# Kernel tuning notes

Measured on AMD Instinct MI355X. Metric: run time of the kernel, lower is better.

The kernel has to match this reference:

```python
import jax, jax.numpy as jnp
import numpy as np

N_NODES = 207
N_EDGES = 1722
N_SLOTS = 288  # 288 / resolution with resolution = 1


def setup_inputs() -> dict:
    key = jax.random.key(0)
    ks = jax.random.split(key, 7)
    B, C, L = 1024, 2, 64
    inputs = jax.random.normal(ks[0], (B, C, N_NODES, L), dtype=jnp.float32)
    weight_diff = jax.random.normal(ks[1], (N_SLOTS, N_EDGES), dtype=jnp.float32) / 1000.0
    bias_diffusion = jax.random.normal(ks[2], (N_SLOTS, N_NODES), dtype=jnp.float32) / 10.0
    weight_self_loop = jax.random.normal(ks[3], (N_SLOTS, N_NODES), dtype=jnp.float32) / 10.0
    ind = jax.random.randint(ks[4], (B,), 0, N_SLOTS, dtype=jnp.int32)
    edge_i = jax.random.randint(ks[5], (N_EDGES,), 0, N_NODES, dtype=jnp.int32)
    edge_j = jax.random.randint(ks[6], (N_EDGES,), 0, N_NODES, dtype=jnp.int32)
    return {"inputs": inputs, "weight_diff": weight_diff,
            "bias_diffusion": bias_diffusion, "weight_self_loop": weight_self_loop,
            "ind": ind, "edge_i": edge_i, "edge_j": edge_j}


def reference(inputs, weight_diff, bias_diffusion, weight_self_loop, ind, edge_i, edge_j):
    # resolution = 1 -> slot index ii == ind
    x = inputs[:, 0, :, :]                      # [B, N, L]
    B, N, _ = x.shape
    w = weight_diff[ind]                        # [B, E] per-sample edge weights
    # symmetric scatter into batched dense adjacency (duplicates sum, as in sparse_coo_tensor)
    A = jnp.zeros((B, N, N), dtype=x.dtype)
    A = A.at[:, edge_i, edge_j].add(w).at[:, edge_j, edge_i].add(w)
    deg = jnp.sum(A, axis=1)                    # [B, N]  (sum over dim 1, as in torch code)
    lap = deg[:, :, None] * jnp.eye(N, dtype=x.dtype) - A  # L = diag(deg) - A
    diffusion = jnp.einsum('nvl,nwv->nwl', x, lap) + bias_diffusion[ind][:, :, None]
    self_loop = weight_self_loop[ind][:, :, None] * x
    return diffusion + x + self_loop
```

## Files before the change

### kernel.cpp

```cpp
#include <hip/hip_runtime.h>
#include <stdint.h>

#define N_NODES 207
#define N_EDGES 1722
#define N_SLOTS 288
#define L_DIM   64
#define EB_STRIDE 4096

__device__ __forceinline__ unsigned int f2bf_rtn_bits_hi(float f) {
    unsigned int u = __float_as_uint(f);
    unsigned int r = u + 0x7FFFu + ((u >> 16) & 1u);
    return r & 0xFFFF0000u;
}

__global__ __launch_bounds__(256) void build_csr_kernel(
    const int* __restrict__ edge_i, const int* __restrict__ edge_j,
    int* __restrict__ rs_p, unsigned int* __restrict__ csr_p) {
    __shared__ int cnt[N_NODES];
    __shared__ int rs[N_NODES + 1];
    const int tid = threadIdx.x;

    for (int n = tid; n < N_NODES; n += 256) cnt[n] = 0;
    __syncthreads();
    for (int e = tid; e < N_EDGES; e += 256) {
        atomicAdd(&cnt[edge_i[e]], 1);
        atomicAdd(&cnt[edge_j[e]], 1);
    }
    __syncthreads();
    if (tid == 0) {
        int acc = 0;
        for (int n = 0; n < N_NODES; ++n) { rs[n] = acc; acc += (cnt[n] + 3) & ~3; }
        rs[N_NODES] = acc;
    }
    __syncthreads();
    for (int n = tid; n <= N_NODES; n += 256) rs_p[n] = rs[n];
    for (int k = tid; k < EB_STRIDE; k += 256) csr_p[k] = 0xFFFFFFFFu;
    for (int n = tid; n < N_NODES; n += 256) cnt[n] = rs[n];
    __syncthreads();
    for (int e = tid; e < N_EDGES; e += 256) {
        const unsigned int i = edge_i[e], j = edge_j[e];
        const unsigned int ep = ((unsigned int)e) << 8;
        int p = atomicAdd(&cnt[i], 1);
        csr_p[p] = ep | j;
        int q = atomicAdd(&cnt[j], 1);
        csr_p[q] = ep | i;
    }
}

__global__ __launch_bounds__(256) void coef_eb_kernel(
    const float* __restrict__ weight_diff, const float* __restrict__ bias_diffusion,
    const float* __restrict__ weight_self_loop,
    const int* __restrict__ rs_p, const unsigned int* __restrict__ csr_p,
    float2* __restrict__ coefbias, unsigned int* __restrict__ eb32p) {
    __shared__ float wrow[N_EDGES];
    const int s = blockIdx.x;
    for (int e = threadIdx.x; e < N_EDGES; e += 256)
        wrow[e] = weight_diff[(size_t)s * N_EDGES + e];
    __syncthreads();

    if (eb32p != nullptr) {
        const int EP = rs_p[N_NODES];
        unsigned int* ebs = eb32p + (size_t)s * EB_STRIDE;
        for (int k = threadIdx.x; k < EB_STRIDE; k += 256) {
            unsigned int v = 0u;
            if (k < EP) {
                const unsigned int c = csr_p[k];
                if (c != 0xFFFFFFFFu)
                    v = f2bf_rtn_bits_hi(wrow[c >> 8]) | ((c & 255u) << 7);
            }
            ebs[k] = v;
        }
    }

    const int n = threadIdx.x;
    if (n < N_NODES) {
        float d = 0.f;
        const int e0 = rs_p[n], e1 = rs_p[n + 1];
        for (int k = e0; k < e1; ++k) {
            const unsigned int c = csr_p[k];
            if (c != 0xFFFFFFFFu) d += wrow[c >> 8];
        }
        coefbias[s * N_NODES + n] = make_float2(
            1.f + weight_self_loop[s * N_NODES + n] + d,
            bias_diffusion[s * N_NODES + n]);
    }
}

__global__ __launch_bounds__(512, 8) void diffusion_quad_kernel(
    const float* __restrict__ inputs,
    const int*   __restrict__ ind,
    const int*   __restrict__ rs_p_g,
    const unsigned int* __restrict__ eb32p,
    const float2* __restrict__ coefbias,
    float* __restrict__ out) {
    __shared__ unsigned short xs[N_NODES * L_DIM];
    __shared__ unsigned int   rsp[N_NODES];

    const int b    = blockIdx.x;
    const int tid  = threadIdx.x;
    const int slot = ind[b];

    const float* xb = inputs + (size_t)b * (2 * N_NODES * L_DIM);

    const float4* xb4 = (const float4*)xb;
    for (int k = tid; k < (N_NODES * L_DIM) / 4; k += 512) {
        const float4 v = xb4[k];
        const unsigned int lo = (f2bf_rtn_bits_hi(v.x) >> 16) | f2bf_rtn_bits_hi(v.y);
        const unsigned int hi = (f2bf_rtn_bits_hi(v.z) >> 16) | f2bf_rtn_bits_hi(v.w);
        ((uint2*)xs)[k] = make_uint2(lo, hi);
    }
    for (int n = tid; n < N_NODES; n += 512)
        rsp[n] = (unsigned int)rs_p_g[n] | ((unsigned int)rs_p_g[n + 1] << 16);
    __syncthreads();

    const int lane = tid & 63;
    const int wv   = tid >> 6;
    const int h    = lane >> 4;
    const unsigned int li8 = (unsigned int)((lane & 15) << 3);
    const unsigned int* ebs = eb32p + (size_t)slot * EB_STRIDE;
    const float2* cbs = coefbias + (size_t)slot * N_NODES;
    float* ob = out + (size_t)b * (N_NODES * L_DIM);
    const char* xsb = (const char*)xs;

    for (int n = wv; n < N_NODES; n += 8) {
        const unsigned int rr = rsp[n];
        const int e0 = (int)(rr & 0xFFFFu);
        const int e1 = (int)(rr >> 16);
        float s0 = 0.f, s1 = 0.f, s2 = 0.f, s3 = 0.f;
        #pragma unroll 2
        for (int k = e0; k < e1; k += 4) {
            const unsigned int p = ebs[k + h];
            const unsigned int w = p & 0xFFFF0000u;
            const unsigned int off = (p & 0xFFFFu) | li8;
            const uint2 xv = *(const uint2*)(xsb + off);
            s0 = fmaf(__uint_as_float(w), __uint_as_float(xv.x << 16), s0);
            s1 = fmaf(__uint_as_float(w), __uint_as_float(xv.x & 0xFFFF0000u), s1);
            s2 = fmaf(__uint_as_float(w), __uint_as_float(xv.y << 16), s2);
            s3 = fmaf(__uint_as_float(w), __uint_as_float(xv.y & 0xFFFF0000u), s3);
        }
        s0 += __shfl_xor(s0, 16); s1 += __shfl_xor(s1, 16);
        s2 += __shfl_xor(s2, 16); s3 += __shfl_xor(s3, 16);
        s0 += __shfl_xor(s0, 32); s1 += __shfl_xor(s1, 32);
        s2 += __shfl_xor(s2, 32); s3 += __shfl_xor(s3, 32);
        if (lane < 16) {
            const float2 cb = cbs[n];
            const int o4 = (n << 6) + (lane << 2);
            const float4 xg = *(const float4*)(xb + o4);
            float4 o;
            o.x = fmaf(cb.x, xg.x, cb.y) - s0;
            o.y = fmaf(cb.x, xg.y, cb.y) - s1;
            o.z = fmaf(cb.x, xg.z, cb.y) - s2;
            o.w = fmaf(cb.x, xg.w, cb.y) - s3;
            *(float4*)(ob + o4) = o;
        }
    }
}

__global__ __launch_bounds__(512, 8) void diffusion_gcn_fallback(
    const float* __restrict__ inputs,
    const float* __restrict__ weight_diff,
    const int*   __restrict__ ind,
    const int*   __restrict__ rs_p_g,
    const unsigned int* __restrict__ csr_p,
    const float2* __restrict__ coefbias,
    float* __restrict__ out) {
    __shared__ unsigned short xsh[N_NODES * L_DIM];
    __shared__ unsigned int   wnb[EB_STRIDE];
    __shared__ unsigned short rs[N_NODES + 1];

    const int b    = blockIdx.x;
    const int tid  = threadIdx.x;
    const int slot = ind[b];

    const float* xb = inputs + (size_t)b * (2 * N_NODES * L_DIM);

    const float4* xb4 = (const float4*)xb;
    for (int k = tid; k < (N_NODES * L_DIM) / 4; k += 512) {
        const float4 v = xb4[k];
        const unsigned int lo = (f2bf_rtn_bits_hi(v.x) >> 16) | f2bf_rtn_bits_hi(v.y);
        const unsigned int hi = (f2bf_rtn_bits_hi(v.z) >> 16) | f2bf_rtn_bits_hi(v.w);
        ((uint2*)xsh)[k] = make_uint2(lo, hi);
    }
    const int EP = rs_p_g[N_NODES];
    const float* wrow = weight_diff + (size_t)slot * N_EDGES;
    for (int k = tid; k < EP; k += 512) {
        const unsigned int c = csr_p[k];
        wnb[k] = (c == 0xFFFFFFFFu) ? 0u
                                    : (f2bf_rtn_bits_hi(wrow[c >> 8]) | (c & 255u));
    }
    for (int n = tid; n <= N_NODES; n += 512) rs[n] = (unsigned short)rs_p_g[n];
    __syncthreads();

    const int lane = tid & 63;
    const int wv   = tid >> 6;
    float* ob = out + (size_t)b * (N_NODES * L_DIM);

    for (int n = wv; n < N_NODES; n += 8) {
        const int e0 = rs[n], e1 = rs[n + 1];
        float s = 0.f;
        #pragma unroll 4
        for (int k = e0; k < e1; ++k) {
            const unsigned int p = wnb[k];
            const float w  = __uint_as_float(p & 0xFFFF0000u);
            const float xv = __uint_as_float(
                (unsigned int)xsh[(p & 255u) * L_DIM + lane] << 16);
            s = fmaf(w, xv, s);
        }
        const float2 cb = coefbias[slot * N_NODES + n];
        const float  xg = xb[n * L_DIM + lane];
        ob[n * L_DIM + lane] = fmaf(cb.x, xg, cb.y) - s;
    }
}

extern "C" void kernel_launch(void* const* d_in, const int* in_sizes, int n_in,
                              void* d_out, int out_size, void* d_ws, size_t ws_size,
                              hipStream_t stream) {
    const float* inputs           = (const float*)d_in[0];
    const float* weight_diff      = (const float*)d_in[1];
    const float* bias_diffusion   = (const float*)d_in[2];
    const float* weight_self_loop = (const float*)d_in[3];
    const int*   ind              = (const int*)d_in[4];
    const int*   edge_i           = (const int*)d_in[5];
    const int*   edge_j           = (const int*)d_in[6];
    float* out = (float*)d_out;

    const int B = in_sizes[4];

    char* ws = (char*)d_ws;
    int*          rs_p     = (int*)ws;
    unsigned int* csr_p    = (unsigned int*)(ws + 1024);
    float2*       coefbias = (float2*)(ws + 17408);
    unsigned int* eb32p    = (unsigned int*)(ws + 494336);
    const size_t WS_FULL = 494336 + (size_t)N_SLOTS * EB_STRIDE * sizeof(unsigned int);

    const bool full = (d_ws != nullptr) && (ws_size >= WS_FULL);

    build_csr_kernel<<<1, 256, 0, stream>>>(edge_i, edge_j, rs_p, csr_p);
    coef_eb_kernel<<<N_SLOTS, 256, 0, stream>>>(
        weight_diff, bias_diffusion, weight_self_loop, rs_p, csr_p,
        coefbias, full ? eb32p : nullptr);
    if (full) {
        diffusion_quad_kernel<<<B, 512, 0, stream>>>(
            inputs, ind, rs_p, eb32p, coefbias, out);
    } else {
        diffusion_gcn_fallback<<<B, 512, 0, stream>>>(
            inputs, weight_diff, ind, rs_p, csr_p, coefbias, out);
    }
}
```

Before: 238.4 us.

## Keep node features in fp32 shared memory and use packed-FMA accumulation

The diffusion kernel now stages the input slice in shared memory as fp32 instead of converting it to bf16. Neighbor rows are read as float4, and accumulation uses 2-wide float vectors so the compiler can emit packed FMA. The edge-buffer node offset is shifted to match the 16-byte row stride. The epilogue also reads x from shared memory instead of global. This removes the bf16 conversion and unpacking ALU work and improves accuracy. In exchange it doubles LDS use (about 53 KB per block), lowers the occupancy hint from 8 to 6, and doubles LDS read bandwidth per edge.

```diff
diff --git a/kernel.cpp b/kernel.cpp
--- a/kernel.cpp
+++ b/kernel.cpp
@@ -6,6 +6,8 @@
 #define N_SLOTS 288
 #define L_DIM   64
 #define EB_STRIDE 4096
+
+typedef __attribute__((ext_vector_type(2))) float f32x2;
 
 __device__ __forceinline__ unsigned int f2bf_rtn_bits_hi(float f) {
     unsigned int u = __float_as_uint(f);
@@ -66,7 +68,7 @@
             if (k < EP) {
                 const unsigned int c = csr_p[k];
                 if (c != 0xFFFFFFFFu)
-                    v = f2bf_rtn_bits_hi(wrow[c >> 8]) | ((c & 255u) << 7);
+                    v = f2bf_rtn_bits_hi(wrow[c >> 8]) | ((c & 255u) << 8);
             }
             ebs[k] = v;
         }
@@ -86,15 +88,15 @@
     }
 }
 
-__global__ __launch_bounds__(512, 8) void diffusion_quad_kernel(
+__global__ __launch_bounds__(512, 6) void diffusion_quad32_kernel(
     const float* __restrict__ inputs,
     const int*   __restrict__ ind,
     const int*   __restrict__ rs_p_g,
     const unsigned int* __restrict__ eb32p,
     const float2* __restrict__ coefbias,
     float* __restrict__ out) {
-    __shared__ unsigned short xs[N_NODES * L_DIM];
-    __shared__ unsigned int   rsp[N_NODES];
+    __shared__ float        xs[N_NODES * L_DIM];
+    __shared__ unsigned int rsp[N_NODES];
 
     const int b    = blockIdx.x;
     const int tid  = threadIdx.x;
@@ -103,12 +105,8 @@
     const float* xb = inputs + (size_t)b * (2 * N_NODES * L_DIM);
 
     const float4* xb4 = (const float4*)xb;
-    for (int k = tid; k < (N_NODES * L_DIM) / 4; k += 512) {
-        const float4 v = xb4[k];
-        const unsigned int lo = (f2bf_rtn_bits_hi(v.x) >> 16) | f2bf_rtn_bits_hi(v.y);
-        const unsigned int hi = (f2bf_rtn_bits_hi(v.z) >> 16) | f2bf_rtn_bits_hi(v.w);
-        ((uint2*)xs)[k] = make_uint2(lo, hi);
-    }
+    float4* xs4 = (float4*)xs;
+    for (int k = tid; k < (N_NODES * L_DIM) / 4; k += 512) xs4[k] = xb4[k];
     for (int n = tid; n < N_NODES; n += 512)
         rsp[n] = (unsigned int)rs_p_g[n] | ((unsigned int)rs_p_g[n + 1] << 16);
     __syncthreads();
@@ -116,8 +114,8 @@
     const int lane = tid & 63;
     const int wv   = tid >> 6;
     const int h    = lane >> 4;
-    const unsigned int li8 = (unsigned int)((lane & 15) << 3);
-    const unsigned int* ebs = eb32p + (size_t)slot * EB_STRIDE;
+    const unsigned int li16 = (unsigned int)((lane & 15) << 4);
+    const unsigned int* ebs = eb32p + (size_t)slot * EB_STRIDE + h;
     const float2* cbs = coefbias + (size_t)slot * N_NODES;
     float* ob = out + (size_t)b * (N_NODES * L_DIM);
     const char* xsb = (const char*)xs;
@@ -126,18 +124,20 @@
         const unsigned int rr = rsp[n];
         const int e0 = (int)(rr & 0xFFFFu);
         const int e1 = (int)(rr >> 16);
-        float s0 = 0.f, s1 = 0.f, s2 = 0.f, s3 = 0.f;
+        f32x2 sA = {0.f, 0.f}, sB = {0.f, 0.f};
         #pragma unroll 2
         for (int k = e0; k < e1; k += 4) {
-            const unsigned int p = ebs[k + h];
-            const unsigned int w = p & 0xFFFF0000u;
-            const unsigned int off = (p & 0xFFFFu) | li8;
-            const uint2 xv = *(const uint2*)(xsb + off);
-            s0 = fmaf(__uint_as_float(w), __uint_as_float(xv.x << 16), s0);
-            s1 = fmaf(__uint_as_float(w), __uint_as_float(xv.x & 0xFFFF0000u), s1);
-            s2 = fmaf(__uint_as_float(w), __uint_as_float(xv.y << 16), s2);
-            s3 = fmaf(__uint_as_float(w), __uint_as_float(xv.y & 0xFFFF0000u), s3);
-        }
+            const unsigned int p = ebs[k];
+            const float w = __uint_as_float(p & 0xFFFF0000u);
+            const unsigned int off = (p & 0xFFFFu) | li16;
+            const float4 xv = *(const float4*)(xsb + off);
+            const f32x2 w2 = {w, w};
+            const f32x2 xlo = {xv.x, xv.y};
+            const f32x2 xhi = {xv.z, xv.w};
+            sA += w2 * xlo;
+            sB += w2 * xhi;
+        }
+        float s0 = sA.x, s1 = sA.y, s2 = sB.x, s3 = sB.y;
         s0 += __shfl_xor(s0, 16); s1 += __shfl_xor(s1, 16);
         s2 += __shfl_xor(s2, 16); s3 += __shfl_xor(s3, 16);
         s0 += __shfl_xor(s0, 32); s1 += __shfl_xor(s1, 32);
@@ -145,7 +145,7 @@
         if (lane < 16) {
             const float2 cb = cbs[n];
             const int o4 = (n << 6) + (lane << 2);
-            const float4 xg = *(const float4*)(xb + o4);
+            const float4 xg = *(const float4*)(xs + o4);
             float4 o;
             o.x = fmaf(cb.x, xg.x, cb.y) - s0;
             o.y = fmaf(cb.x, xg.y, cb.y) - s1;
@@ -240,7 +240,7 @@
         weight_diff, bias_diffusion, weight_self_loop, rs_p, csr_p,
         coefbias, full ? eb32p : nullptr);
     if (full) {
-        diffusion_quad_kernel<<<B, 512, 0, stream>>>(
+        diffusion_quad32_kernel<<<B, 512, 0, stream>>>(
             inputs, ind, rs_p, eb32p, coefbias, out);
     } else {
         diffusion_gcn_fallback<<<B, 512, 0, stream>>>(
```

Result: slower. 255.1 us (+7.0%).

## Flatten per-wave edge groups with shared-memory bf16 weights and topology

Applied to the files above, without the earlier changes.

Builds a per-wave flattened edge layout in which nodes are padded to groups of four and assigned round-robin to the eight waves. A node-id array marks group boundaries. Per-slot weights are stored as 16-bit bf16 values, separate from an 8-bit neighbor topology array. The diffusion kernel stages weights, topology and node ids into LDS and runs one continuous loop per wave, reducing and writing output whenever the node changes. This aims to remove per-node loop overhead and the global 32-bit edge-word loads, at the cost of more LDS use (which may lower occupancy) and a divergent reduction branch inside the inner loop.

```diff
diff --git a/kernel.cpp b/kernel.cpp
--- a/kernel.cpp
+++ b/kernel.cpp
@@ -5,19 +5,27 @@
 #define N_EDGES 1722
 #define N_SLOTS 288
 #define L_DIM   64
-#define EB_STRIDE 4096
+#define CSRP_CAP 4096
+#define WSTR_CAP 4608
+#define W16_STRIDE 4608
+#define NGRP_CAP 1280
 
 __device__ __forceinline__ unsigned int f2bf_rtn_bits_hi(float f) {
     unsigned int u = __float_as_uint(f);
     unsigned int r = u + 0x7FFFu + ((u >> 16) & 1u);
     return r & 0xFFFF0000u;
 }
+__device__ __forceinline__ float uf(unsigned int u) { return __uint_as_float(u); }
 
 __global__ __launch_bounds__(256) void build_csr_kernel(
     const int* __restrict__ edge_i, const int* __restrict__ edge_j,
-    int* __restrict__ rs_p, unsigned int* __restrict__ csr_p) {
+    int* __restrict__ rs_p, unsigned int* __restrict__ csr_p,
+    unsigned int* __restrict__ csr_w, unsigned char* __restrict__ topo8,
+    unsigned char* __restrict__ nodearr, int* __restrict__ wvoff) {
     __shared__ int cnt[N_NODES];
     __shared__ int rs[N_NODES + 1];
+    __shared__ int nbase[N_NODES];
+    __shared__ int ngsz[N_NODES];
     const int tid = threadIdx.x;
 
     for (int n = tid; n < N_NODES; n += 256) cnt[n] = 0;
@@ -34,7 +42,7 @@
     }
     __syncthreads();
     for (int n = tid; n <= N_NODES; n += 256) rs_p[n] = rs[n];
-    for (int k = tid; k < EB_STRIDE; k += 256) csr_p[k] = 0xFFFFFFFFu;
+    for (int k = tid; k < CSRP_CAP; k += 256) csr_p[k] = 0xFFFFFFFFu;
     for (int n = tid; n < N_NODES; n += 256) cnt[n] = rs[n];
     __syncthreads();
     for (int e = tid; e < N_EDGES; e += 256) {
@@ -45,30 +53,65 @@
         int q = atomicAdd(&cnt[j], 1);
         csr_p[q] = ep | i;
     }
+    __syncthreads();
+    if (tid == 0) {
+        int wsz[8] = {0,0,0,0,0,0,0,0};
+        for (int n = 0; n < N_NODES; ++n) {
+            int dp = rs[n + 1] - rs[n];
+            int g = (dp > 4) ? dp : 4;
+            ngsz[n] = g;
+            wsz[n & 7] += g;
+        }
+        int acc = 0, wo[9];
+        for (int w = 0; w < 8; ++w) { wo[w] = acc; acc += wsz[w]; }
+        wo[8] = acc;
+        for (int w = 0; w <= 8; ++w) wvoff[w] = wo[w];
+        int cur[8];
+        for (int w = 0; w < 8; ++w) cur[w] = wo[w];
+        for (int n = 0; n < N_NODES; ++n) {
+            const int w = n & 7;
+            nbase[n] = cur[w];
+            cur[w] += ngsz[n];
+        }
+        nodearr[acc >> 2] = 0xFFu;
+    }
+    __syncthreads();
+    for (int n = tid; n < N_NODES; n += 256) {
+        const int b0 = nbase[n], dp = rs[n + 1] - rs[n], g = ngsz[n];
+        for (int i = 0; i < dp; ++i) {
+            const unsigned int c = csr_p[rs[n] + i];
+            csr_w[b0 + i] = c;
+            topo8[b0 + i] = (unsigned char)(c & 255u);
+        }
+        for (int i = dp; i < g; ++i) {
+            csr_w[b0 + i] = 0xFFFFFFFFu;
+            topo8[b0 + i] = 0;
+        }
+        const int G = g >> 2, gb = b0 >> 2;
+        for (int j = 0; j < G; ++j) nodearr[gb + j] = (unsigned char)n;
+    }
 }
 
 __global__ __launch_bounds__(256) void coef_eb_kernel(
     const float* __restrict__ weight_diff, const float* __restrict__ bias_diffusion,
     const float* __restrict__ weight_self_loop,
     const int* __restrict__ rs_p, const unsigned int* __restrict__ csr_p,
-    float2* __restrict__ coefbias, unsigned int* __restrict__ eb32p) {
+    const unsigned int* __restrict__ csr_w, const int* __restrict__ wvoff,
+    float2* __restrict__ coefbias, unsigned short* __restrict__ w16) {
     __shared__ float wrow[N_EDGES];
     const int s = blockIdx.x;
     for (int e = threadIdx.x; e < N_EDGES; e += 256)
         wrow[e] = weight_diff[(size_t)s * N_EDGES + e];
     __syncthreads();
 
-    if (eb32p != nullptr) {
-        const int EP = rs_p[N_NODES];
-        unsigned int* ebs = eb32p + (size_t)s * EB_STRIDE;
-        for (int k = threadIdx.x; k < EB_STRIDE; k += 256) {
-            unsigned int v = 0u;
-            if (k < EP) {
-                const unsigned int c = csr_p[k];
-                if (c != 0xFFFFFFFFu)
-                    v = f2bf_rtn_bits_hi(wrow[c >> 8]) | ((c & 255u) << 7);
-            }
-            ebs[k] = v;
+    if (w16 != nullptr) {
+        const int total = wvoff[8];
+        unsigned short* ws = w16 + (size_t)s * W16_STRIDE;
+        for (int k = threadIdx.x; k < total; k += 256) {
+            const unsigned int c = csr_w[k];
+            ws[k] = (c == 0xFFFFFFFFu)
+                  ? (unsigned short)0
+                  : (unsigned short)(f2bf_rtn_bits_hi(wrow[c >> 8]) >> 16);
         }
     }
 
@@ -86,19 +129,24 @@
     }
 }
 
-__global__ __launch_bounds__(512, 8) void diffusion_quad_kernel(
+__global__ __launch_bounds__(512, 8) void diffusion_flat_kernel(
     const float* __restrict__ inputs,
     const int*   __restrict__ ind,
-    const int*   __restrict__ rs_p_g,
-    const unsigned int* __restrict__ eb32p,
+    const int*   __restrict__ wvoff,
+    const unsigned char*  __restrict__ topo8,
+    const unsigned char*  __restrict__ nodearr,
+    const unsigned short* __restrict__ w16,
     const float2* __restrict__ coefbias,
     float* __restrict__ out) {
     __shared__ unsigned short xs[N_NODES * L_DIM];
-    __shared__ unsigned int   rsp[N_NODES];
+    __shared__ unsigned short ws16[WSTR_CAP - 256];
+    __shared__ unsigned char  tp[WSTR_CAP - 256];
+    __shared__ unsigned char  ndl[1152];
 
     const int b    = blockIdx.x;
     const int tid  = threadIdx.x;
     const int slot = ind[b];
+    const int total = wvoff[8];
 
     const float* xb = inputs + (size_t)b * (2 * N_NODES * L_DIM);
 
@@ -109,54 +157,65 @@
         const unsigned int hi = (f2bf_rtn_bits_hi(v.z) >> 16) | f2bf_rtn_bits_hi(v.w);
         ((uint2*)xs)[k] = make_uint2(lo, hi);
     }
-    for (int n = tid; n < N_NODES; n += 512)
-        rsp[n] = (unsigned int)rs_p_g[n] | ((unsigned int)rs_p_g[n + 1] << 16);
+    {
+        const unsigned int* wg = (const unsigned int*)(w16 + (size_t)slot * W16_STRIDE);
+        for (int k = tid; k < (total >> 1); k += 512) ((unsigned int*)ws16)[k] = wg[k];
+        const unsigned int* tg = (const unsigned int*)topo8;
+        for (int k = tid; k < (total >> 2); k += 512) ((unsigned int*)tp)[k] = tg[k];
+        const unsigned int* ng = (const unsigned int*)nodearr;
+        const int ngw = ((total >> 2) + 1 + 3) >> 2;
+        for (int k = tid; k < ngw; k += 512) ((unsigned int*)ndl)[k] = ng[k];
+    }
     __syncthreads();
 
     const int lane = tid & 63;
     const int wv   = tid >> 6;
     const int h    = lane >> 4;
     const unsigned int li8 = (unsigned int)((lane & 15) << 3);
-    const unsigned int* ebs = eb32p + (size_t)slot * EB_STRIDE;
     const float2* cbs = coefbias + (size_t)slot * N_NODES;
     float* ob = out + (size_t)b * (N_NODES * L_DIM);
     const char* xsb = (const char*)xs;
 
-    for (int n = wv; n < N_NODES; n += 8) {
-        const unsigned int rr = rsp[n];
-        const int e0 = (int)(rr & 0xFFFFu);
-        const int e1 = (int)(rr >> 16);
-        float s0 = 0.f, s1 = 0.f, s2 = 0.f, s3 = 0.f;
-        #pragma unroll 2
-        for (int k = e0; k < e1; k += 4) {
-            const unsigned int p = ebs[k + h];
-            const unsigned int w = p & 0xFFFF0000u;
-            const unsigned int off = (p & 0xFFFFu) | li8;
-            const uint2 xv = *(const uint2*)(xsb + off);
-            s0 = fmaf(__uint_as_float(w), __uint_as_float(xv.x << 16), s0);
-            s1 = fmaf(__uint_as_float(w), __uint_as_float(xv.x & 0xFFFF0000u), s1);
-            s2 = fmaf(__uint_as_float(w), __uint_as_float(xv.y << 16), s2);
-            s3 = fmaf(__uint_as_float(w), __uint_as_float(xv.y & 0xFFFF0000u), s3);
-        }
-        s0 += __shfl_xor(s0, 16); s1 += __shfl_xor(s1, 16);
-        s2 += __shfl_xor(s2, 16); s3 += __shfl_xor(s3, 16);
-        s0 += __shfl_xor(s0, 32); s1 += __shfl_xor(s1, 32);
-        s2 += __shfl_xor(s2, 32); s3 += __shfl_xor(s3, 32);
-        if (lane < 16) {
-            const float2 cb = cbs[n];
-            const int o4 = (n << 6) + (lane << 2);
-            const float4 xg = *(const float4*)(xb + o4);
-            float4 o;
-            o.x = fmaf(cb.x, xg.x, cb.y) - s0;
-            o.y = fmaf(cb.x, xg.y, cb.y) - s1;
-            o.z = fmaf(cb.x, xg.z, cb.y) - s2;
-            o.w = fmaf(cb.x, xg.w, cb.y) - s3;
-            *(float4*)(ob + o4) = o;
-        }
-    }
-}
-
-__global__ __launch_bounds__(512, 8) void diffusion_gcn_fallback(
+    const int g0 = wvoff[wv] >> 2;
+    const int g1 = wvoff[wv + 1] >> 2;
+    float s0 = 0.f, s1 = 0.f, s2 = 0.f, s3 = 0.f;
+    unsigned int nCur = ndl[g0];
+    #pragma unroll 2
+    for (int g = g0; g < g1; ++g) {
+        const unsigned int nNext = ndl[g + 1];
+        const int e = (g << 2) + h;
+        const unsigned int wbits = ((unsigned int)ws16[e]) << 16;
+        const unsigned int off = ((unsigned int)tp[e] << 7) | li8;
+        const uint2 xv = *(const uint2*)(xsb + off);
+        s0 = fmaf(uf(wbits), uf(xv.x << 16),         s0);
+        s1 = fmaf(uf(wbits), uf(xv.x & 0xFFFF0000u), s1);
+        s2 = fmaf(uf(wbits), uf(xv.y << 16),         s2);
+        s3 = fmaf(uf(wbits), uf(xv.y & 0xFFFF0000u), s3);
+        if (nNext != nCur) {
+            float r0 = s0, r1 = s1, r2 = s2, r3 = s3;
+            r0 += __shfl_xor(r0, 16); r1 += __shfl_xor(r1, 16);
+            r2 += __shfl_xor(r2, 16); r3 += __shfl_xor(r3, 16);
+            r0 += __shfl_xor(r0, 32); r1 += __shfl_xor(r1, 32);
+            r2 += __shfl_xor(r2, 32); r3 += __shfl_xor(r3, 32);
+            if (lane < 16) {
+                const int n = (int)nCur;
+                const float2 cb = cbs[n];
+                const int o4 = (n << 6) + (lane << 2);
+                const float4 xg = *(const float4*)(xb + o4);
+                float4 o;
+                o.x = fmaf(cb.x, xg.x, cb.y) - r0;
+                o.y = fmaf(cb.x, xg.y, cb.y) - r1;
+                o.z = fmaf(cb.x, xg.z, cb.y) - r2;
+                o.w = fmaf(cb.x, xg.w, cb.y) - r3;
+                *(float4*)(ob + o4) = o;
+            }
+            s0 = s1 = s2 = s3 = 0.f;
+            nCur = nNext;
+        }
+    }
+}
+
+__global__ __launch_bounds__(512, 4) void diffusion_gcn_fallback(
     const float* __restrict__ inputs,
     const float* __restrict__ weight_diff,
     const int*   __restrict__ ind,
@@ -165,7 +224,7 @@
     const float2* __restrict__ coefbias,
     float* __restrict__ out) {
     __shared__ unsigned short xsh[N_NODES * L_DIM];
-    __shared__ unsigned int   wnb[EB_STRIDE];
+    __shared__ unsigned int   wnb[CSRP_CAP];
     __shared__ unsigned short rs[N_NODES + 1];
 
     const int b    = blockIdx.x;
@@ -227,21 +286,26 @@
     const int B = in_sizes[4];
 
     char* ws = (char*)d_ws;
-    int*          rs_p     = (int*)ws;
-    unsigned int* csr_p    = (unsigned int*)(ws + 1024);
-    float2*       coefbias = (float2*)(ws + 17408);
-    unsigned int* eb32p    = (unsigned int*)(ws + 494336);
-    const size_t WS_FULL = 494336 + (size_t)N_SLOTS * EB_STRIDE * sizeof(unsigned int);
+    int*            rs_p     = (int*)ws;
+    unsigned int*   csr_p    = (unsigned int*)(ws + 1024);
+    unsigned int*   csr_w    = (unsigned int*)(ws + 17408);
+    unsigned char*  topo8    = (unsigned char*)(ws + 35840);
+    unsigned char*  nodearr  = (unsigned char*)(ws + 40448);
+    int*            wvoff    = (int*)(ws + 41728);
+    float2*         coefbias = (float2*)(ws + 41792);
+    unsigned short* w16      = (unsigned short*)(ws + 518720);
+    const size_t WS_FULL = 518720 + (size_t)N_SLOTS * W16_STRIDE * sizeof(unsigned short);
 
     const bool full = (d_ws != nullptr) && (ws_size >= WS_FULL);
 
-    build_csr_kernel<<<1, 256, 0, stream>>>(edge_i, edge_j, rs_p, csr_p);
+    build_csr_kernel<<<1, 256, 0, stream>>>(
+        edge_i, edge_j, rs_p, csr_p, csr_w, topo8, nodearr, wvoff);
     coef_eb_kernel<<<N_SLOTS, 256, 0, stream>>>(
-        weight_diff, bias_diffusion, weight_self_loop, rs_p, csr_p,
-        coefbias, full ? eb32p : nullptr);
+        weight_diff, bias_diffusion, weight_self_loop, rs_p, csr_p, csr_w, wvoff,
+        coefbias, full ? w16 : nullptr);
     if (full) {
-        diffusion_quad_kernel<<<B, 512, 0, stream>>>(
-            inputs, ind, rs_p, eb32p, coefbias, out);
+        diffusion_flat_kernel<<<B, 512, 0, stream>>>(
+            inputs, ind, wvoff, topo8, nodearr, w16, coefbias, out);
     } else {
         diffusion_gcn_fallback<<<B, 512, 0, stream>>>(
             inputs, weight_diff, ind, rs_p, csr_p, coefbias, out);
```

Measured after the change: 274.3 us. 15.0% more time.

## Replace per-node CSR loop with interleaved 32-stream edge schedule per quarter-wave

Applied to the files above, without the earlier changes.

Builds a node-interleaved edge stream in which each of 32 quarter-wave streams walks the neighbour lists of every 32nd node back to back. End-of-row flags tell the stream when to emit an output. Per-slot packed weights are laid out column-major across streams, so each quarter-wave reads coalesced entries with a two-deep prefetch, and the shuffle reductions and padded-to-4 loop structure go away. The trade is that streams are padded to the longest stream length T, which is capped at 256 and could silently truncate work for denser graphs. The fallback kernel's occupancy hint also changes.

```diff
diff --git a/kernel.cpp b/kernel.cpp
--- a/kernel.cpp
+++ b/kernel.cpp
@@ -5,19 +5,28 @@
 #define N_EDGES 1722
 #define N_SLOTS 288
 #define L_DIM   64
-#define EB_STRIDE 4096
+#define CSRP_CAP 4096
+#define T_CAP   256
+#define T_ROWS  (T_CAP + 2)
+#define SLOT_U32 (32 * T_ROWS)
 
 __device__ __forceinline__ unsigned int f2bf_rtn_bits_hi(float f) {
     unsigned int u = __float_as_uint(f);
     unsigned int r = u + 0x7FFFu + ((u >> 16) & 1u);
     return r & 0xFFFF0000u;
 }
+__device__ __forceinline__ float uf(unsigned int u) { return __uint_as_float(u); }
 
 __global__ __launch_bounds__(256) void build_csr_kernel(
     const int* __restrict__ edge_i, const int* __restrict__ edge_j,
-    int* __restrict__ rs_p, unsigned int* __restrict__ csr_p) {
+    int* __restrict__ rs_p, unsigned int* __restrict__ csr_p,
+    unsigned int* __restrict__ m32, int* __restrict__ stream_T) {
     __shared__ int cnt[N_NODES];
     __shared__ int rs[N_NODES + 1];
+    __shared__ int scnt[N_NODES];
+    __shared__ int nsbase[N_NODES];
+    __shared__ int slen[32];
+    __shared__ int sT;
     const int tid = threadIdx.x;
 
     for (int n = tid; n < N_NODES; n += 256) cnt[n] = 0;
@@ -34,7 +43,7 @@
     }
     __syncthreads();
     for (int n = tid; n <= N_NODES; n += 256) rs_p[n] = rs[n];
-    for (int k = tid; k < EB_STRIDE; k += 256) csr_p[k] = 0xFFFFFFFFu;
+    for (int k = tid; k < CSRP_CAP; k += 256) csr_p[k] = 0xFFFFFFFFu;
     for (int n = tid; n < N_NODES; n += 256) cnt[n] = rs[n];
     __syncthreads();
     for (int e = tid; e < N_EDGES; e += 256) {
@@ -45,30 +54,70 @@
         int q = atomicAdd(&cnt[j], 1);
         csr_p[q] = ep | i;
     }
+    __syncthreads();
+    for (int n = tid; n < N_NODES; n += 256) scnt[n] = cnt[n];
+    __syncthreads();
+    if (tid == 0) {
+        int T = 0;
+        for (int q = 0; q < 32; ++q) {
+            int off = 0;
+            for (int n = q; n < N_NODES; n += 32) {
+                nsbase[n] = off;
+                const int deg = scnt[n] - rs[n];
+                off += (deg > 0) ? deg : 1;
+            }
+            slen[q] = off;
+            if (off > T) T = off;
+        }
+        if (T > T_CAP) T = T_CAP;
+        sT = T;
+        stream_T[0] = T;
+    }
+    __syncthreads();
+    const int T2 = sT + 2;
+    for (int n = tid; n < N_NODES; n += 256) {
+        const int q = n & 31;
+        const int deg = scnt[n] - rs[n];
+        if (deg == 0) {
+            if (nsbase[n] < T2) m32[nsbase[n] * 32 + q] = (2047u << 9) | 1u;
+        } else {
+            for (int i = 0; i < deg; ++i) {
+                const int t = nsbase[n] + i;
+                if (t >= T2) break;
+                const unsigned int c = csr_p[rs[n] + i];
+                const unsigned int fl = (i == deg - 1) ? 1u : 0u;
+                m32[t * 32 + q] = ((c >> 8) << 9) | ((c & 255u) << 1) | fl;
+            }
+        }
+    }
+    for (int idx = tid; idx < 32 * T2; idx += 256) {
+        const int t = idx >> 5, q = idx & 31;
+        if (t >= slen[q]) m32[t * 32 + q] = (2047u << 9);
+    }
 }
 
 __global__ __launch_bounds__(256) void coef_eb_kernel(
     const float* __restrict__ weight_diff, const float* __restrict__ bias_diffusion,
     const float* __restrict__ weight_self_loop,
     const int* __restrict__ rs_p, const unsigned int* __restrict__ csr_p,
-    float2* __restrict__ coefbias, unsigned int* __restrict__ eb32p) {
+    const unsigned int* __restrict__ m32, const int* __restrict__ stream_T,
+    float2* __restrict__ coefbias, unsigned int* __restrict__ p32) {
     __shared__ float wrow[N_EDGES];
     const int s = blockIdx.x;
     for (int e = threadIdx.x; e < N_EDGES; e += 256)
         wrow[e] = weight_diff[(size_t)s * N_EDGES + e];
     __syncthreads();
 
-    if (eb32p != nullptr) {
-        const int EP = rs_p[N_NODES];
-        unsigned int* ebs = eb32p + (size_t)s * EB_STRIDE;
-        for (int k = threadIdx.x; k < EB_STRIDE; k += 256) {
-            unsigned int v = 0u;
-            if (k < EP) {
-                const unsigned int c = csr_p[k];
-                if (c != 0xFFFFFFFFu)
-                    v = f2bf_rtn_bits_hi(wrow[c >> 8]) | ((c & 255u) << 7);
-            }
-            ebs[k] = v;
+    if (p32 != nullptr) {
+        const int total = 32 * (stream_T[0] + 2);
+        unsigned int* ps = p32 + (size_t)s * SLOT_U32;
+        for (int k = threadIdx.x; k < total; k += 256) {
+            const unsigned int m = m32[k];
+            const unsigned int eid = m >> 9;
+            const unsigned int nb  = (m >> 1) & 255u;
+            const unsigned int fl  = m & 1u;
+            const unsigned int w16 = (eid < N_EDGES) ? f2bf_rtn_bits_hi(wrow[eid]) : 0u;
+            ps[k] = w16 | (nb << 7) | fl;
         }
     }
 
@@ -86,19 +135,19 @@
     }
 }
 
-__global__ __launch_bounds__(512, 8) void diffusion_quad_kernel(
+__global__ __launch_bounds__(512, 8) void diffusion_stream_kernel(
     const float* __restrict__ inputs,
     const int*   __restrict__ ind,
-    const int*   __restrict__ rs_p_g,
-    const unsigned int* __restrict__ eb32p,
+    const int*   __restrict__ stream_T,
+    const unsigned int* __restrict__ p32,
     const float2* __restrict__ coefbias,
     float* __restrict__ out) {
     __shared__ unsigned short xs[N_NODES * L_DIM];
-    __shared__ unsigned int   rsp[N_NODES];
 
     const int b    = blockIdx.x;
     const int tid  = threadIdx.x;
     const int slot = ind[b];
+    const int T    = stream_T[0];
 
     const float* xb = inputs + (size_t)b * (2 * N_NODES * L_DIM);
 
@@ -109,54 +158,52 @@
         const unsigned int hi = (f2bf_rtn_bits_hi(v.z) >> 16) | f2bf_rtn_bits_hi(v.w);
         ((uint2*)xs)[k] = make_uint2(lo, hi);
     }
-    for (int n = tid; n < N_NODES; n += 512)
-        rsp[n] = (unsigned int)rs_p_g[n] | ((unsigned int)rs_p_g[n + 1] << 16);
     __syncthreads();
 
     const int lane = tid & 63;
     const int wv   = tid >> 6;
-    const int h    = lane >> 4;
+    const int q    = (wv << 2) | (lane >> 4);
+    const int i4   = (lane & 15) << 2;
     const unsigned int li8 = (unsigned int)((lane & 15) << 3);
-    const unsigned int* ebs = eb32p + (size_t)slot * EB_STRIDE;
+    const unsigned int* ebs = p32 + (size_t)slot * SLOT_U32 + q;
     const float2* cbs = coefbias + (size_t)slot * N_NODES;
     float* ob = out + (size_t)b * (N_NODES * L_DIM);
     const char* xsb = (const char*)xs;
 
-    for (int n = wv; n < N_NODES; n += 8) {
-        const unsigned int rr = rsp[n];
-        const int e0 = (int)(rr & 0xFFFFu);
-        const int e1 = (int)(rr >> 16);
-        float s0 = 0.f, s1 = 0.f, s2 = 0.f, s3 = 0.f;
-        #pragma unroll 2
-        for (int k = e0; k < e1; k += 4) {
-            const unsigned int p = ebs[k + h];
-            const unsigned int w = p & 0xFFFF0000u;
-            const unsigned int off = (p & 0xFFFFu) | li8;
-            const uint2 xv = *(const uint2*)(xsb + off);
-            s0 = fmaf(__uint_as_float(w), __uint_as_float(xv.x << 16), s0);
-            s1 = fmaf(__uint_as_float(w), __uint_as_float(xv.x & 0xFFFF0000u), s1);
-            s2 = fmaf(__uint_as_float(w), __uint_as_float(xv.y << 16), s2);
-            s3 = fmaf(__uint_as_float(w), __uint_as_float(xv.y & 0xFFFF0000u), s3);
-        }
-        s0 += __shfl_xor(s0, 16); s1 += __shfl_xor(s1, 16);
-        s2 += __shfl_xor(s2, 16); s3 += __shfl_xor(s3, 16);
-        s0 += __shfl_xor(s0, 32); s1 += __shfl_xor(s1, 32);
-        s2 += __shfl_xor(s2, 32); s3 += __shfl_xor(s3, 32);
-        if (lane < 16) {
-            const float2 cb = cbs[n];
-            const int o4 = (n << 6) + (lane << 2);
-            const float4 xg = *(const float4*)(xb + o4);
+    int n = q;
+    float2 cb = cbs[n];
+    float4 xg = *(const float4*)(xb + (n << 6) + i4);
+    float s0 = 0.f, s1 = 0.f, s2 = 0.f, s3 = 0.f;
+    unsigned int p0 = ebs[0];
+    unsigned int p1 = ebs[32];
+    for (int t = 0; t < T; ++t) {
+        const unsigned int p2 = ebs[(t + 2) << 5];
+        const unsigned int p = p0;
+        const uint2 xv = *(const uint2*)(xsb + ((p & 0x7F80u) | li8));
+        const unsigned int w = p & 0xFFFF0000u;
+        s0 = fmaf(uf(w), uf(xv.x << 16),         s0);
+        s1 = fmaf(uf(w), uf(xv.x & 0xFFFF0000u), s1);
+        s2 = fmaf(uf(w), uf(xv.y << 16),         s2);
+        s3 = fmaf(uf(w), uf(xv.y & 0xFFFF0000u), s3);
+        if (p & 1u) {
             float4 o;
             o.x = fmaf(cb.x, xg.x, cb.y) - s0;
             o.y = fmaf(cb.x, xg.y, cb.y) - s1;
             o.z = fmaf(cb.x, xg.z, cb.y) - s2;
             o.w = fmaf(cb.x, xg.w, cb.y) - s3;
-            *(float4*)(ob + o4) = o;
-        }
-    }
-}
-
-__global__ __launch_bounds__(512, 8) void diffusion_gcn_fallback(
+            *(float4*)(ob + (n << 6) + i4) = o;
+            s0 = s1 = s2 = s3 = 0.f;
+            n += 32;
+            if (n < N_NODES) {
+                cb = cbs[n];
+                xg = *(const float4*)(xb + (n << 6) + i4);
+            }
+        }
+        p0 = p1; p1 = p2;
+    }
+}
+
+__global__ __launch_bounds__(512, 6) void diffusion_gcn_fallback(
     const float* __restrict__ inputs,
     const float* __restrict__ weight_diff,
     const int*   __restrict__ ind,
@@ -165,7 +212,7 @@
     const float2* __restrict__ coefbias,
     float* __restrict__ out) {
     __shared__ unsigned short xsh[N_NODES * L_DIM];
-    __shared__ unsigned int   wnb[EB_STRIDE];
+    __shared__ unsigned int   wnb[CSRP_CAP];
     __shared__ unsigned short rs[N_NODES + 1];
 
     const int b    = blockIdx.x;
@@ -229,19 +276,22 @@
     char* ws = (char*)d_ws;
     int*          rs_p     = (int*)ws;
     unsigned int* csr_p    = (unsigned int*)(ws + 1024);
-    float2*       coefbias = (float2*)(ws + 17408);
-    unsigned int* eb32p    = (unsigned int*)(ws + 494336);
-    const size_t WS_FULL = 494336 + (size_t)N_SLOTS * EB_STRIDE * sizeof(unsigned int);
+    int*          stream_T = (int*)(ws + 17408);
+    unsigned int* m32      = (unsigned int*)(ws + 17472);
+    float2*       coefbias = (float2*)(ws + 50496);
+    unsigned int* p32      = (unsigned int*)(ws + 527424);
+    const size_t WS_FULL = 527424 + (size_t)N_SLOTS * SLOT_U32 * sizeof(unsigned int);
 
     const bool full = (d_ws != nullptr) && (ws_size >= WS_FULL);
 
-    build_csr_kernel<<<1, 256, 0, stream>>>(edge_i, edge_j, rs_p, csr_p);
+    build_csr_kernel<<<1, 256, 0, stream>>>(
+        edge_i, edge_j, rs_p, csr_p, m32, stream_T);
     coef_eb_kernel<<<N_SLOTS, 256, 0, stream>>>(
-        weight_diff, bias_diffusion, weight_self_loop, rs_p, csr_p,
-        coefbias, full ? eb32p : nullptr);
+        weight_diff, bias_diffusion, weight_self_loop, rs_p, csr_p, m32, stream_T,
+        coefbias, full ? p32 : nullptr);
     if (full) {
-        diffusion_quad_kernel<<<B, 512, 0, stream>>>(
-            inputs, ind, rs_p, eb32p, coefbias, out);
+        diffusion_stream_kernel<<<B, 512, 0, stream>>>(
+            inputs, ind, stream_T, p32, coefbias, out);
     } else {
         diffusion_gcn_fallback<<<B, 512, 0, stream>>>(
             inputs, weight_diff, ind, rs_p, csr_p, coefbias, out);
```

Measured after the change: 241.1 us. No clear change (+1.1%).
